# Kernel optimization log

Measured on AMD Instinct MI355X. Metric: run time of the kernel, lower is better.

## Reference

```python
import jax, jax.numpy as jnp
import numpy as np

HID = 2048      # hidden_size
INTER = 8192    # intermediate_size
QKV = 8192      # lin_qkv_dim
TV = 4096       # lin_total_val
NVH = 32        # lin_num_val_heads
KD = 128        # lin_key_dim
VD = 128        # lin_val_dim
NKH = 16        # lin_num_key_heads
CK = 4          # conv_kernel
RATIO = NVH // NKH
EPS = 1e-6


def setup_inputs() -> dict:
    key = jax.random.key(0)
    ks = jax.random.split(key, 16)
    s = 0.02
    return dict(
        x=jax.random.normal(ks[0], (1, HID), dtype=jnp.float32),
        conv_state=jax.random.normal(ks[1], (QKV, CK), dtype=jnp.float32),
        ssm_state=jax.random.normal(ks[2], (NVH, KD, VD), dtype=jnp.float32) * 0.1,
        in_ln_w=jax.random.normal(ks[3], (HID,), dtype=jnp.float32) * s,
        in_proj_w=jax.random.normal(ks[4], (QKV + TV + 2 * NVH, HID), dtype=jnp.float32) * s,
        conv_w=jax.random.normal(ks[5], (QKV, CK), dtype=jnp.float32) * s,
        A_log=jax.random.normal(ks[6], (NVH,), dtype=jnp.float32) * s,
        dt_bias=jax.random.normal(ks[7], (NVH,), dtype=jnp.float32) * s,
        norm_w=jnp.ones((VD,), dtype=jnp.float32) + jax.random.normal(ks[8], (VD,), dtype=jnp.float32) * s,
        out_proj_w=jax.random.normal(ks[9], (HID, TV), dtype=jnp.float32) * s,
        post_ln_w=jax.random.normal(ks[10], (HID,), dtype=jnp.float32) * s,
        gate_w=jax.random.normal(ks[11], (INTER, HID), dtype=jnp.float32) * s,
        up_w=jax.random.normal(ks[12], (INTER, HID), dtype=jnp.float32) * s,
        down_w=jax.random.normal(ks[13], (HID, INTER), dtype=jnp.float32) * s,
    )


def _rmsnorm(x, w, eps=EPS):
    # Qwen3.5-style: scale applied as (1 + w)
    var = jnp.mean(jnp.square(x), axis=-1, keepdims=True)
    return x * jax.lax.rsqrt(var + eps) * (1.0 + w)


def _l2norm(x, eps=1e-12):
    # matches torch F.normalize(p=2): x / max(||x||, eps)
    n = jnp.sqrt(jnp.sum(jnp.square(x), axis=-1, keepdims=True))
    return x / jnp.maximum(n, eps)


def reference(x, conv_state, ssm_state, in_ln_w, in_proj_w, conv_w, A_log,
              dt_bias, norm_w, out_proj_w, post_ln_w, gate_w, up_w, down_w):
    residual = x
    h = _rmsnorm(x, in_ln_w)
    proj = h @ in_proj_w.T                         # [1, QKV+TV+2*NVH]
    mixed_qkv = proj[:, :QKV]
    z = proj[:, QKV:QKV + TV]
    ab = proj[:, QKV + TV:]
    a_raw = ab[:, :NVH]
    b_raw = ab[:, NVH:]

    # depthwise causal conv buffer update + conv step
    new_conv_state = jnp.concatenate([conv_state[:, 1:], mixed_qkv.reshape(QKV, 1)], axis=1)
    conv_out = jax.nn.silu(jnp.sum(new_conv_state * conv_w, axis=1))  # [QKV]

    key_total = NKH * KD
    q = conv_out[:key_total].reshape(NKH, KD)
    k = conv_out[key_total:2 * key_total].reshape(NKH, KD)
    v = conv_out[2 * key_total:].reshape(NVH, VD)
    q = jnp.repeat(q, RATIO, axis=0)               # [NVH, KD]
    k = jnp.repeat(k, RATIO, axis=0)
    q = _l2norm(q)
    k = _l2norm(k)

    beta = jax.nn.sigmoid(b_raw[0])                # [NVH]
    g = -jnp.exp(A_log) * jax.nn.softplus(a_raw[0] + dt_bias)
    decay = jnp.exp(g)                             # [NVH]

    # delta-rule state update
    Sk = jnp.einsum('hkv,hk->hv', ssm_state, k)    # [NVH, VD]
    delta = v - Sk
    outer = k[:, :, None] * delta[:, None, :]      # [NVH, KD, VD]
    new_ssm_state = decay[:, None, None] * ssm_state + beta[:, None, None] * outer
    y = jnp.einsum('hkv,hk->hv', new_ssm_state, q) # [NVH, VD]

    # per-head gated RMSNorm (plain weight, not 1+w)
    var = jnp.mean(jnp.square(y), axis=-1, keepdims=True)
    y_norm = y * jax.lax.rsqrt(var + 1e-6) * norm_w[None, :]
    z_r = z.reshape(NVH, VD)
    y_gated = (y_norm * jax.nn.silu(z_r)).reshape(1, TV)

    attn_out = y_gated @ out_proj_w.T              # [1, HID]
    x1 = residual + attn_out

    # SwiGLU FFN with pre-norm
    hn = _rmsnorm(x1, post_ln_w)
    ffn = (jax.nn.silu(hn @ gate_w.T) * (hn @ up_w.T)) @ down_w.T
    x_out = x1 + ffn
    return (x_out, new_conv_state, new_ssm_state)
```

## Files before the change

kernel.cpp:

```cpp
#include <hip/hip_runtime.h>
#include <hip/hip_bf16.h>

#define HID 2048
#define INTER 8192
#define QKV 8192
#define TV 4096
#define NVH 32
#define KD 128
#define VD 128
#define NKH 16
#define CK 4
#define NPROJ (QKV + TV + 2*NVH)

__device__ __forceinline__ float wave_sum(float v){
#pragma unroll
  for (int off = 32; off > 0; off >>= 1) v += __shfl_down(v, off, 64);
  return v;
}

__global__ void rmsnorm_kernel(const float* __restrict__ x, const float* __restrict__ w,
                               float* __restrict__ out){
  int t = threadIdx.x;
  float xs[8];
  float s = 0.f;
#pragma unroll
  for (int i = 0; i < 8; i++){ float v = x[t + i*256]; xs[i] = v; s += v*v; }
  __shared__ float red[4];
  float ps = wave_sum(s);
  if ((t & 63) == 0) red[t >> 6] = ps;
  __syncthreads();
  float tot = red[0] + red[1] + red[2] + red[3];
  float inv = rsqrtf(tot / (float)HID + 1e-6f);
#pragma unroll
  for (int i = 0; i < 8; i++){
    int idx = t + i*256;
    out[idx] = xs[i] * inv * (1.f + w[idx]);
  }
}

__global__ void in_proj_kernel(const float* __restrict__ W, const float* __restrict__ h,
                               const float* __restrict__ conv_state, const float* __restrict__ conv_w,
                               float* __restrict__ conv_out, float* __restrict__ z,
                               float* __restrict__ ab, float* __restrict__ new_conv_state){
  int row  = blockIdx.x * 4 + (threadIdx.x >> 6);
  int lane = threadIdx.x & 63;
  const float4* W4 = (const float4*)W + (size_t)row * (HID/4);
  const float4* h4 = (const float4*)h;
  float acc = 0.f;
#pragma unroll
  for (int c = 0; c < HID/4/64; c++){
    float4 a = W4[c*64 + lane];
    float4 b = h4[c*64 + lane];
    acc += a.x*b.x + a.y*b.y + a.z*b.z + a.w*b.w;
  }
  acc = wave_sum(acc);
  if (lane == 0){
    if (row < QKV){
      float c1 = conv_state[row*4+1], c2 = conv_state[row*4+2], c3 = conv_state[row*4+3];
      const float4 cw = ((const float4*)conv_w)[row];
      float s = c1*cw.x + c2*cw.y + c3*cw.z + acc*cw.w;
      conv_out[row] = s / (1.f + expf(-s));
      ((float4*)new_conv_state)[row] = make_float4(c1, c2, c3, acc);
    } else if (row < QKV + TV){
      z[row - QKV] = acc;
    } else {
      ab[row - (QKV + TV)] = acc;
    }
  }
}

__global__ void ssm_kernel(const float* __restrict__ S, const float* __restrict__ conv_out,
                           const float* __restrict__ z, const float* __restrict__ ab,
                           const float* __restrict__ A_log, const float* __restrict__ dt_bias,
                           const float* __restrict__ norm_w,
                           float* __restrict__ newS, float* __restrict__ y_gated){
  int hh = blockIdx.x;
  int t  = threadIdx.x;
  int v  = t & 127;
  int half = t >> 7;
  __shared__ float s_q[KD], s_k[KD], sP[256], redq[4], redk[4], redy[4];

  float qr = 0.f, kr = 0.f;
  if (t < KD){
    int kvh = hh >> 1;
    qr = conv_out[kvh*KD + t];
    kr = conv_out[NKH*KD + kvh*KD + t];
  }
  float q2 = wave_sum(qr*qr);
  float k2 = wave_sum(kr*kr);
  if ((t & 63) == 0){ redq[t>>6] = q2; redk[t>>6] = k2; }
  __syncthreads();
  float qs = redq[0]+redq[1]+redq[2]+redq[3];
  float ks = redk[0]+redk[1]+redk[2]+redk[3];
  if (t < KD){
    s_q[t] = qr / fmaxf(sqrtf(qs), 1e-12f);
    s_k[t] = kr / fmaxf(sqrtf(ks), 1e-12f);
  }
  __syncthreads();

  float a     = ab[hh] + dt_bias[hh];
  float sp    = log1pf(expf(a));
  float decay = expf(-expf(A_log[hh]) * sp);
  float beta  = 1.f / (1.f + expf(-ab[NVH + hh]));

  const float* Sh  = S    + (size_t)hh * KD * VD;
  float*       nSh = newS + (size_t)hh * KD * VD;
  int k0 = half * 64;

  float acc = 0.f;
#pragma unroll 8
  for (int kk = 0; kk < 64; kk++)
    acc += Sh[(k0+kk)*VD + v] * s_k[k0+kk];
  sP[t] = acc;
  __syncthreads();
  float Sk    = sP[v] + sP[128 + v];
  float vv    = conv_out[2*NKH*KD + hh*VD + v];
  float delta = vv - Sk;
  __syncthreads();

  float y = 0.f;
#pragma unroll 8
  for (int kk = 0; kk < 64; kk++){
    int krow = k0 + kk;
    float ns = decay * Sh[krow*VD + v] + beta * s_k[krow] * delta;
    nSh[krow*VD + v] = ns;
    y += ns * s_q[krow];
  }
  sP[t] = y;
  __syncthreads();
  float yv = 0.f;
  if (t < VD) yv = sP[t] + sP[128 + t];
  float y2 = wave_sum(yv*yv);
  if ((t & 63) == 0) redy[t>>6] = y2;
  __syncthreads();
  float var = (redy[0]+redy[1]+redy[2]+redy[3]) / (float)VD;
  if (t < VD){
    float yn = yv * rsqrtf(var + 1e-6f) * norm_w[t];
    float zz = z[hh*VD + t];
    y_gated[hh*VD + t] = yn * (zz / (1.f + expf(-zz)));
  }
}

__global__ void out_proj_kernel(const float* __restrict__ W, const float* __restrict__ yg,
                                const float* __restrict__ x, float* __restrict__ x1){
  int row  = blockIdx.x * 4 + (threadIdx.x >> 6);
  int lane = threadIdx.x & 63;
  const float4* W4 = (const float4*)W + (size_t)row * (TV/4);
  const float4* g4 = (const float4*)yg;
  float acc = 0.f;
#pragma unroll
  for (int c = 0; c < TV/4/64; c++){
    float4 a = W4[c*64 + lane];
    float4 b = g4[c*64 + lane];
    acc += a.x*b.x + a.y*b.y + a.z*b.z + a.w*b.w;
  }
  acc = wave_sum(acc);
  if (lane == 0) x1[row] = x[row] + acc;
}

__global__ void gateup_kernel(const float* __restrict__ Wg, const float* __restrict__ Wu,
                              const float* __restrict__ hn, float* __restrict__ inter){
  int row  = blockIdx.x * 4 + (threadIdx.x >> 6);
  int lane = threadIdx.x & 63;
  const float4* G4 = (const float4*)Wg + (size_t)row * (HID/4);
  const float4* U4 = (const float4*)Wu + (size_t)row * (HID/4);
  const float4* h4 = (const float4*)hn;
  float g = 0.f, u = 0.f;
#pragma unroll
  for (int c = 0; c < HID/4/64; c++){
    float4 b = h4[c*64 + lane];
    float4 a = G4[c*64 + lane];
    g += a.x*b.x + a.y*b.y + a.z*b.z + a.w*b.w;
    float4 e = U4[c*64 + lane];
    u += e.x*b.x + e.y*b.y + e.z*b.z + e.w*b.w;
  }
  g = wave_sum(g);
  u = wave_sum(u);
  if (lane == 0) inter[row] = (g / (1.f + expf(-g))) * u;
}

__global__ void down_kernel(const float* __restrict__ W, const float* __restrict__ inter,
                            const float* __restrict__ x1, float* __restrict__ out){
  int row  = blockIdx.x * 4 + (threadIdx.x >> 6);
  int lane = threadIdx.x & 63;
  const float4* W4 = (const float4*)W + (size_t)row * (INTER/4);
  const float4* i4 = (const float4*)inter;
  float acc = 0.f;
#pragma unroll
  for (int c = 0; c < INTER/4/64; c++){
    float4 a = W4[c*64 + lane];
    float4 b = i4[c*64 + lane];
    acc += a.x*b.x + a.y*b.y + a.z*b.z + a.w*b.w;
  }
  acc = wave_sum(acc);
  if (lane == 0) out[row] = x1[row] + acc;
}

extern "C" void kernel_launch(void* const* d_in, const int* in_sizes, int n_in,
                              void* d_out, int out_size, void* d_ws, size_t ws_size,
                              hipStream_t stream) {
  const float* x         = (const float*)d_in[0];
  const float* conv_st   = (const float*)d_in[1];
  const float* ssm_st    = (const float*)d_in[2];
  const float* in_ln_w   = (const float*)d_in[3];
  const float* in_proj_w = (const float*)d_in[4];
  const float* conv_w    = (const float*)d_in[5];
  const float* A_log     = (const float*)d_in[6];
  const float* dt_bias   = (const float*)d_in[7];
  const float* norm_w    = (const float*)d_in[8];
  const float* out_proj_w= (const float*)d_in[9];
  const float* post_ln_w = (const float*)d_in[10];
  const float* gate_w    = (const float*)d_in[11];
  const float* up_w      = (const float*)d_in[12];
  const float* down_w    = (const float*)d_in[13];

  float* out_x   = (float*)d_out;
  float* out_cs  = out_x + HID;
  float* out_ssm = out_cs + QKV*CK;

  float* ws       = (float*)d_ws;
  float* h        = ws;
  float* conv_out = h + HID;
  float* z        = conv_out + QKV;
  float* ab       = z + TV;
  float* y_gated  = ab + 64;
  float* x1       = y_gated + TV;
  float* hn       = x1 + HID;
  float* inter    = hn + HID;

  rmsnorm_kernel <<<1,         256, 0, stream>>>(x, in_ln_w, h);
  in_proj_kernel <<<NPROJ/4,   256, 0, stream>>>(in_proj_w, h, conv_st, conv_w,
                                                 conv_out, z, ab, out_cs);
  ssm_kernel     <<<NVH,       256, 0, stream>>>(ssm_st, conv_out, z, ab, A_log, dt_bias,
                                                 norm_w, out_ssm, y_gated);
  out_proj_kernel<<<HID/4,     256, 0, stream>>>(out_proj_w, y_gated, x, x1);
  rmsnorm_kernel <<<1,         256, 0, stream>>>(x1, post_ln_w, hn);
  gateup_kernel  <<<INTER/4,   256, 0, stream>>>(gate_w, up_w, hn, inter);
  down_kernel    <<<HID/4,     256, 0, stream>>>(down_w, inter, x1, out_x);
}
```

Before: 343.0 us.

## Fuse RMSNorms into projection kernels and cache SSM state in registers

Both single-block RMSNorm launches are removed. Every block of the in_proj and gate/up GEMV kernels now recomputes the norm of the 2048-element vector into LDS, which eliminates two serialized tiny launches and the global round trips for h and hn. The SSM kernel keeps each thread's 64 state values in registers, so the state is read from global memory once instead of twice. Unroll factors and launch bounds are also adjusted. In exchange, each of thousands of blocks repeats the norm work and adds a block barrier, and the 64-entry register array raises register pressure.

```diff
diff --git a/kernel.cpp b/kernel.cpp
--- a/kernel.cpp
+++ b/kernel.cpp
@@ -18,34 +18,38 @@
   return v;
 }
 
-__global__ void rmsnorm_kernel(const float* __restrict__ x, const float* __restrict__ w,
-                               float* __restrict__ out){
+__device__ __forceinline__ void rmsnorm_to_lds(const float* __restrict__ src,
+                                               const float* __restrict__ w,
+                                               float* s_h, float* red){
   int t = threadIdx.x;
-  float xs[8];
-  float s = 0.f;
-#pragma unroll
-  for (int i = 0; i < 8; i++){ float v = x[t + i*256]; xs[i] = v; s += v*v; }
-  __shared__ float red[4];
+  float xs[8]; float s = 0.f;
+#pragma unroll
+  for (int i = 0; i < 8; i++){ float v = src[t + i*256]; xs[i] = v; s += v*v; }
   float ps = wave_sum(s);
   if ((t & 63) == 0) red[t >> 6] = ps;
   __syncthreads();
-  float tot = red[0] + red[1] + red[2] + red[3];
-  float inv = rsqrtf(tot / (float)HID + 1e-6f);
+  float inv = rsqrtf((red[0]+red[1]+red[2]+red[3]) / (float)HID + 1e-6f);
 #pragma unroll
   for (int i = 0; i < 8; i++){
     int idx = t + i*256;
-    out[idx] = xs[i] * inv * (1.f + w[idx]);
-  }
-}
-
-__global__ void in_proj_kernel(const float* __restrict__ W, const float* __restrict__ h,
-                               const float* __restrict__ conv_state, const float* __restrict__ conv_w,
-                               float* __restrict__ conv_out, float* __restrict__ z,
-                               float* __restrict__ ab, float* __restrict__ new_conv_state){
+    s_h[idx] = xs[i] * inv * (1.f + w[idx]);
+  }
+  __syncthreads();
+}
+
+__global__ __launch_bounds__(256) void in_proj_fused(
+    const float* __restrict__ x, const float* __restrict__ ln_w,
+    const float* __restrict__ W, const float* __restrict__ conv_state,
+    const float* __restrict__ conv_w, float* __restrict__ conv_out,
+    float* __restrict__ z, float* __restrict__ ab, float* __restrict__ new_conv_state){
+  __shared__ __align__(16) float s_h[HID];
+  __shared__ float red[4];
+  rmsnorm_to_lds(x, ln_w, s_h, red);
+
   int row  = blockIdx.x * 4 + (threadIdx.x >> 6);
   int lane = threadIdx.x & 63;
   const float4* W4 = (const float4*)W + (size_t)row * (HID/4);
-  const float4* h4 = (const float4*)h;
+  const float4* h4 = (const float4*)s_h;
   float acc = 0.f;
 #pragma unroll
   for (int c = 0; c < HID/4/64; c++){
@@ -69,11 +73,12 @@
   }
 }
 
-__global__ void ssm_kernel(const float* __restrict__ S, const float* __restrict__ conv_out,
-                           const float* __restrict__ z, const float* __restrict__ ab,
-                           const float* __restrict__ A_log, const float* __restrict__ dt_bias,
-                           const float* __restrict__ norm_w,
-                           float* __restrict__ newS, float* __restrict__ y_gated){
+__global__ __launch_bounds__(256) void ssm_kernel(
+    const float* __restrict__ S, const float* __restrict__ conv_out,
+    const float* __restrict__ z, const float* __restrict__ ab,
+    const float* __restrict__ A_log, const float* __restrict__ dt_bias,
+    const float* __restrict__ norm_w,
+    float* __restrict__ newS, float* __restrict__ y_gated){
   int hh = blockIdx.x;
   int t  = threadIdx.x;
   int v  = t & 127;
@@ -107,10 +112,13 @@
   float*       nSh = newS + (size_t)hh * KD * VD;
   int k0 = half * 64;
 
-  float acc = 0.f;
-#pragma unroll 8
-  for (int kk = 0; kk < 64; kk++)
-    acc += Sh[(k0+kk)*VD + v] * s_k[k0+kk];
+  float sreg[64];
+  float acc = 0.f;
+#pragma unroll
+  for (int kk = 0; kk < 64; kk++){
+    sreg[kk] = Sh[(k0+kk)*VD + v];
+    acc += sreg[kk] * s_k[k0+kk];
+  }
   sP[t] = acc;
   __syncthreads();
   float Sk    = sP[v] + sP[128 + v];
@@ -119,10 +127,10 @@
   __syncthreads();
 
   float y = 0.f;
-#pragma unroll 8
+#pragma unroll
   for (int kk = 0; kk < 64; kk++){
     int krow = k0 + kk;
-    float ns = decay * Sh[krow*VD + v] + beta * s_k[krow] * delta;
+    float ns = decay * sreg[kk] + beta * s_k[krow] * delta;
     nSh[krow*VD + v] = ns;
     y += ns * s_q[krow];
   }
@@ -141,14 +149,15 @@
   }
 }
 
-__global__ void out_proj_kernel(const float* __restrict__ W, const float* __restrict__ yg,
-                                const float* __restrict__ x, float* __restrict__ x1){
+__global__ __launch_bounds__(256) void out_proj_kernel(
+    const float* __restrict__ W, const float* __restrict__ yg,
+    const float* __restrict__ x, float* __restrict__ x1){
   int row  = blockIdx.x * 4 + (threadIdx.x >> 6);
   int lane = threadIdx.x & 63;
   const float4* W4 = (const float4*)W + (size_t)row * (TV/4);
   const float4* g4 = (const float4*)yg;
   float acc = 0.f;
-#pragma unroll
+#pragma unroll 8
   for (int c = 0; c < TV/4/64; c++){
     float4 a = W4[c*64 + lane];
     float4 b = g4[c*64 + lane];
@@ -158,15 +167,21 @@
   if (lane == 0) x1[row] = x[row] + acc;
 }
 
-__global__ void gateup_kernel(const float* __restrict__ Wg, const float* __restrict__ Wu,
-                              const float* __restrict__ hn, float* __restrict__ inter){
+__global__ __launch_bounds__(256) void gateup_fused(
+    const float* __restrict__ x1, const float* __restrict__ ln_w,
+    const float* __restrict__ Wg, const float* __restrict__ Wu,
+    float* __restrict__ inter){
+  __shared__ __align__(16) float s_h[HID];
+  __shared__ float red[4];
+  rmsnorm_to_lds(x1, ln_w, s_h, red);
+
   int row  = blockIdx.x * 4 + (threadIdx.x >> 6);
   int lane = threadIdx.x & 63;
   const float4* G4 = (const float4*)Wg + (size_t)row * (HID/4);
   const float4* U4 = (const float4*)Wu + (size_t)row * (HID/4);
-  const float4* h4 = (const float4*)hn;
+  const float4* h4 = (const float4*)s_h;
   float g = 0.f, u = 0.f;
-#pragma unroll
+#pragma unroll 4
   for (int c = 0; c < HID/4/64; c++){
     float4 b = h4[c*64 + lane];
     float4 a = G4[c*64 + lane];
@@ -179,14 +194,15 @@
   if (lane == 0) inter[row] = (g / (1.f + expf(-g))) * u;
 }
 
-__global__ void down_kernel(const float* __restrict__ W, const float* __restrict__ inter,
-                            const float* __restrict__ x1, float* __restrict__ out){
+__global__ __launch_bounds__(256) void down_kernel(
+    const float* __restrict__ W, const float* __restrict__ inter,
+    const float* __restrict__ x1, float* __restrict__ out){
   int row  = blockIdx.x * 4 + (threadIdx.x >> 6);
   int lane = threadIdx.x & 63;
   const float4* W4 = (const float4*)W + (size_t)row * (INTER/4);
   const float4* i4 = (const float4*)inter;
   float acc = 0.f;
-#pragma unroll
+#pragma unroll 8
   for (int c = 0; c < INTER/4/64; c++){
     float4 a = W4[c*64 + lane];
     float4 b = i4[c*64 + lane];
@@ -219,22 +235,18 @@
   float* out_ssm = out_cs + QKV*CK;
 
   float* ws       = (float*)d_ws;
-  float* h        = ws;
-  float* conv_out = h + HID;
+  float* conv_out = ws;
   float* z        = conv_out + QKV;
   float* ab       = z + TV;
   float* y_gated  = ab + 64;
   float* x1       = y_gated + TV;
-  float* hn       = x1 + HID;
-  float* inter    = hn + HID;
-
-  rmsnorm_kernel <<<1,         256, 0, stream>>>(x, in_ln_w, h);
-  in_proj_kernel <<<NPROJ/4,   256, 0, stream>>>(in_proj_w, h, conv_st, conv_w,
-                                                 conv_out, z, ab, out_cs);
-  ssm_kernel     <<<NVH,       256, 0, stream>>>(ssm_st, conv_out, z, ab, A_log, dt_bias,
-                                                 norm_w, out_ssm, y_gated);
-  out_proj_kernel<<<HID/4,     256, 0, stream>>>(out_proj_w, y_gated, x, x1);
-  rmsnorm_kernel <<<1,         256, 0, stream>>>(x1, post_ln_w, hn);
-  gateup_kernel  <<<INTER/4,   256, 0, stream>>>(gate_w, up_w, hn, inter);
-  down_kernel    <<<HID/4,     256, 0, stream>>>(down_w, inter, x1, out_x);
-}
+  float* inter    = x1 + HID;
+
+  in_proj_fused  <<<NPROJ/4,  256, 0, stream>>>(x, in_ln_w, in_proj_w, conv_st, conv_w,
+                                                conv_out, z, ab, out_cs);
+  ssm_kernel     <<<NVH,      256, 0, stream>>>(ssm_st, conv_out, z, ab, A_log, dt_bias,
+                                                norm_w, out_ssm, y_gated);
+  out_proj_kernel<<<HID/4,    256, 0, stream>>>(out_proj_w, y_gated, x, x1);
+  gateup_fused   <<<INTER/4,  256, 0, stream>>>(x1, post_ln_w, gate_w, up_w, inter);
+  down_kernel    <<<HID/4,    256, 0, stream>>>(down_w, inter, x1, out_x);
+}
```

Result: faster. 331.3 us (-3.4%).
